# Performance work log

Measured on AMD Instinct MI355X. Metric: run time of the kernel, lower is better.

## Reference

```python
import jax, jax.numpy as jnp
import numpy as np

NUM_EMBEDDINGS = 1024
EMBEDDING_DIM = 64
COMMITMENT_COST = 0.25


def setup_inputs() -> dict:
    key = jax.random.key(0)
    k1, k2 = jax.random.split(key)
    inputs = jax.random.normal(k1, (32, 4096, EMBEDDING_DIM), dtype=jnp.float32)
    lim = 1.0 / NUM_EMBEDDINGS
    embedding = jax.random.uniform(k2, (NUM_EMBEDDINGS, EMBEDDING_DIM),
                                   dtype=jnp.float32, minval=-lim, maxval=lim)
    return {"inputs": inputs, "embedding": embedding}


def reference(inputs, embedding):
    input_shape = inputs.shape
    flat = inputs.reshape(-1, EMBEDDING_DIM)                     # [N, D]
    # Squared euclidean distances via the expanded form (same math as torch cdist trick)
    distances = (jnp.sum(flat ** 2, axis=1, keepdims=True)
                 + jnp.sum(embedding ** 2, axis=1)
                 - 2.0 * flat @ embedding.T)                     # [N, K]
    encoding_indices = jnp.argmin(distances, axis=1)             # [N]
    # one-hot @ embedding == gather of nearest code rows
    quantized = embedding[encoding_indices].reshape(input_shape)
    e_latent_loss = jnp.mean((jax.lax.stop_gradient(quantized) - inputs) ** 2)
    q_latent_loss = jnp.mean((quantized - jax.lax.stop_gradient(inputs)) ** 2)
    loss = q_latent_loss + COMMITMENT_COST * e_latent_loss
    # straight-through estimator
    quantized_st = inputs + jax.lax.stop_gradient(quantized - inputs)
    return loss, quantized_st, encoding_indices[:, None]
```

## Files before the change

### kernel.cpp

```cpp
#include <hip/hip_runtime.h>

#define D 64
#define K 1024
#define NROWS (32 * 4096)
#define NELEM (NROWS * D)
#define COMMIT 0.25f
#define DELTA 1.2e-4f
#define HDELTA 6e-5f
#define RPB 128
#define CHUNK 128
#define EPAD 68

typedef __attribute__((ext_vector_type(8))) short short8v;
typedef __attribute__((ext_vector_type(4))) float f32x4;
typedef unsigned long long u64;

#define FORSLOT8(M) M(0) M(1) M(2) M(3) M(4) M(5) M(6) M(7)

static __device__ __forceinline__ float fence(float v) {
    asm("" : "+v"(v));
    return v;
}

static __device__ __forceinline__ unsigned short f2bf(float f) {
    unsigned u = __float_as_uint(f);
    return (unsigned short)((u + 0x7FFFu + ((u >> 16) & 1u)) >> 16);
}

static __device__ __forceinline__ float np_sumsq64(const float* __restrict__ e) {
    float r[8];
#pragma unroll
    for (int j = 0; j < 8; ++j) r[j] = fence(e[j] * e[j]);
#pragma unroll
    for (int t = 1; t < 8; ++t)
#pragma unroll
        for (int j = 0; j < 8; ++j) r[j] = r[j] + fence(e[8 * t + j] * e[8 * t + j]);
    return ((r[0] + r[1]) + (r[2] + r[3])) + ((r[4] + r[5]) + (r[6] + r[7]));
}

static __device__ __forceinline__ float exact_score(
    const float* __restrict__ xrow, const float* __restrict__ erow, float R,
    float N) {
    float a = 0.0f;
#pragma unroll
    for (int i = 0; i < D; ++i) a = __builtin_fmaf(xrow[i], erow[i], a);
    return (R + N) - 2.0f * a;
}

__global__ void prep_emb_kernel(const float* __restrict__ emb,
                                float* __restrict__ enorm,
                                float* __restrict__ enorm_nh,
                                unsigned short* __restrict__ e_hi,
                                float* __restrict__ loss_slot) {
    int k = blockIdx.x * blockDim.x + threadIdx.x;
    if (k == 0) *loss_slot = 0.0f;
    if (k >= K) return;
    float n = np_sumsq64(emb + k * D);
    enorm[k] = n;
    enorm_nh[k] = -0.5f * n;
    const float* e = emb + k * D;
#pragma unroll
    for (int i = 0; i < D; ++i) e_hi[k * D + i] = f2bf(e[i]);
}

__global__ __launch_bounds__(256, 1) void argmin_kernel(
    const float* __restrict__ x, const float* __restrict__ emb,
    const float* __restrict__ enorm, const float* __restrict__ enorm_nh,
    const unsigned short* __restrict__ e_hi, float* __restrict__ out_q,
    float* __restrict__ idx_f, float* __restrict__ loss_slot) {
    const int tid = threadIdx.x;
    const int l = tid & 63;
    const int w = tid >> 6;
    const int col = l & 15;
    const int koff = (l >> 4) * 8;
    const int blockrow = blockIdx.x * RPB;
    const int wrow = blockrow + w * 32;

    __shared__ unsigned short eB[CHUNK * EPAD];
    __shared__ float nB[CHUNK];
    __shared__ int cnt[RPB];
    __shared__ int clist[RPB][4];
    __shared__ int bidx[RPB];
    __shared__ float wsum[4];

#define DECL_A(rt, h)                                                       \
    short8v Ahi_##rt##_##h;                                                 \
    { const float* p = x + (size_t)(wrow + rt * 16 + col) * D + h * 32 + koff; \
      float4 q0 = *(const float4*)p, q1 = *(const float4*)(p + 4);          \
      Ahi_##rt##_##h[0] = (short)f2bf(q0.x);                                \
      Ahi_##rt##_##h[1] = (short)f2bf(q0.y);                                \
      Ahi_##rt##_##h[2] = (short)f2bf(q0.z);                                \
      Ahi_##rt##_##h[3] = (short)f2bf(q0.w);                                \
      Ahi_##rt##_##h[4] = (short)f2bf(q1.x);                                \
      Ahi_##rt##_##h[5] = (short)f2bf(q1.y);                                \
      Ahi_##rt##_##h[6] = (short)f2bf(q1.z);                                \
      Ahi_##rt##_##h[7] = (short)f2bf(q1.w); }
    DECL_A(0, 0) DECL_A(0, 1) DECL_A(1, 0) DECL_A(1, 1)

#define SLOTROW(s) (((s) / 4) * 16 + (l >> 4) * 4 + ((s) % 4))

#define STAGE(c)                                                            \
    {                                                                       \
        _Pragma("unroll")                                                   \
        for (int i = 0; i < 4; ++i) {                                       \
            int G = tid + i * 256;                 \
            int cd = G >> 3, wi = G & 7;                                    \
            *(short8v*)(&eB[cd * EPAD + wi * 8]) =                          \
                *(const short8v*)(e_hi +                                    \
                    (((size_t)((c) * CHUNK + cd)) << 6) + wi * 8);          \
        }                                                                   \
        if (tid < CHUNK) nB[tid] = enorm_nh[(c) * CHUNK + tid];             \
    }

#define DECL_MA(s) float mA_##s = -3.402823466e+38f;
    FORSLOT8(DECL_MA)
#define MFMA2A(rt, sA, sB, sC, sD)                                          \
    { f32x4 acc = {Nc, Nc, Nc, Nc};                                         \
      acc = __builtin_amdgcn_mfma_f32_16x16x32_bf16(Ahi_##rt##_0, Bhi0, acc, 0, 0, 0); \
      acc = __builtin_amdgcn_mfma_f32_16x16x32_bf16(Ahi_##rt##_1, Bhi1, acc, 0, 0, 0); \
      mA_##sA = fmaxf(mA_##sA, acc[0]);                                     \
      mA_##sB = fmaxf(mA_##sB, acc[1]);                                     \
      mA_##sC = fmaxf(mA_##sC, acc[2]);                                     \
      mA_##sD = fmaxf(mA_##sD, acc[3]); }
    for (int c = 0; c < 8; ++c) {
        __syncthreads();
        STAGE(c)
        __syncthreads();
#pragma unroll 2
        for (int nt = 0; nt < 8; ++nt) {
            const int cc = nt * 16 + col;
            const short8v Bhi0 = *(const short8v*)(&eB[cc * EPAD + koff]);
            const short8v Bhi1 = *(const short8v*)(&eB[cc * EPAD + 32 + koff]);
            const float Nc = nB[cc];
            MFMA2A(0, 0, 1, 2, 3) MFMA2A(1, 4, 5, 6, 7)
        }
    }
#define BFA(s)                                                              \
    mA_##s = fmaxf(mA_##s, __shfl_xor(mA_##s, 1));                          \
    mA_##s = fmaxf(mA_##s, __shfl_xor(mA_##s, 2));                          \
    mA_##s = fmaxf(mA_##s, __shfl_xor(mA_##s, 4));                          \
    mA_##s = fmaxf(mA_##s, __shfl_xor(mA_##s, 8));
    FORSLOT8(BFA)
#define DECL_T(s) const float thr_##s = mA_##s - HDELTA;
    FORSLOT8(DECL_T)
    if (tid < RPB) cnt[tid] = 0;

#define CHK(s, av)                                                          \
    { if ((av) >= thr_##s) {                                                \
          int row = w * 32 + SLOTROW(s);                                    \
          int pos = atomicAdd(&cnt[row], 1);                                \
          if (pos < 4) clist[row][pos] = code;                              \
      } }
#define MFMA2B(rt, sA, sB, sC, sD)                                          \
    { f32x4 acc = {Nc, Nc, Nc, Nc};                                         \
      acc = __builtin_amdgcn_mfma_f32_16x16x32_bf16(Ahi_##rt##_0, Bhi0, acc, 0, 0, 0); \
      acc = __builtin_amdgcn_mfma_f32_16x16x32_bf16(Ahi_##rt##_1, Bhi1, acc, 0, 0, 0); \
      CHK(sA, acc[0]) CHK(sB, acc[1]) CHK(sC, acc[2]) CHK(sD, acc[3]) }
    for (int c = 0; c < 8; ++c) {
        __syncthreads();
        STAGE(c)
        __syncthreads();
#pragma unroll 2
        for (int nt = 0; nt < 8; ++nt) {
            const int cc = nt * 16 + col;
            const short8v Bhi0 = *(const short8v*)(&eB[cc * EPAD + koff]);
            const short8v Bhi1 = *(const short8v*)(&eB[cc * EPAD + 32 + koff]);
            const float Nc = nB[cc];
            const int code = c * CHUNK + cc;
            MFMA2B(0, 0, 1, 2, 3) MFMA2B(1, 4, 5, 6, 7)
        }
    }
    __syncthreads();

    if (tid < RPB) {
        const int row = tid;
        const int n = cnt[row];
        int bk;
        if (n == 1) {
            bk = clist[row][0];
        } else {
            const float* xrow = x + (size_t)(blockrow + row) * D;
            const float R = np_sumsq64(xrow);
            float sb = 3.402823466e+38f;
            int kb = 0x7fffffff;
            if (n <= 4) {
                for (int i = 0; i < n; ++i) {
                    int c = clist[row][i];
                    float s = exact_score(xrow, emb + ((size_t)c << 6), R,
                                          enorm[c]);
                    if (s < sb || (s == sb && c < kb)) { sb = s; kb = c; }
                }
            } else {
                for (int c = 0; c < K; ++c) {
                    float s = exact_score(xrow, emb + ((size_t)c << 6), R,
                                          enorm[c]);
                    if (s < sb || (s == sb && c < kb)) { sb = s; kb = c; }
                }
            }
            bk = kb;
        }
        bidx[row] = bk;
        idx_f[blockrow + row] = (float)bk;
    }
    __syncthreads();

    float lsum = 0.f;
#pragma unroll
    for (int rr = 0; rr < 2; ++rr) {
        const int row = rr * 64 + (tid >> 2);
        const int d0 = (tid & 3) * 16;
        const int bk = bidx[row];
        const float4* xq =
            (const float4*)(x + (size_t)(blockrow + row) * D + d0);
        const float4* eq = (const float4*)(emb + ((size_t)bk << 6) + d0);
        float4* oq = (float4*)(out_q + (size_t)(blockrow + row) * D + d0);
#pragma unroll
        for (int i = 0; i < 4; ++i) {
            float4 xv = xq[i];
            float4 ev = eq[i];
            float dx = ev.x - xv.x, dy = ev.y - xv.y, dz = ev.z - xv.z,
                  dw = ev.w - xv.w;
            float4 o;
            o.x = xv.x + dx;
            o.y = xv.y + dy;
            o.z = xv.z + dz;
            o.w = xv.w + dw;
            oq[i] = o;
            lsum = __builtin_fmaf(dx, dx, lsum);
            lsum = __builtin_fmaf(dy, dy, lsum);
            lsum = __builtin_fmaf(dz, dz, lsum);
            lsum = __builtin_fmaf(dw, dw, lsum);
        }
    }
#pragma unroll
    for (int o = 32; o > 0; o >>= 1) lsum += __shfl_xor(lsum, o);
    if (l == 0) wsum[w] = lsum;
    __syncthreads();
    if (tid == 0)
        atomicAdd(loss_slot, ((wsum[0] + wsum[1]) + (wsum[2] + wsum[3])) *
                                 ((1.0f + COMMIT) / (float)NELEM));
}

extern "C" void kernel_launch(void* const* d_in, const int* in_sizes, int n_in,
                              void* d_out, int out_size, void* d_ws,
                              size_t ws_size, hipStream_t stream) {
    const float* x = (const float*)d_in[0];
    const float* emb = (const float*)d_in[1];

    float* out = (float*)d_out;
    float* loss_slot = out;
    float* out_q = out + 1;
    float* idx_f = out + 1 + NELEM;

    float* enorm = (float*)d_ws;
    float* enorm_nh = (float*)((char*)d_ws + 4096);
    unsigned short* e_hi = (unsigned short*)((char*)d_ws + 8192);

    prep_emb_kernel<<<(K + 255) / 256, 256, 0, stream>>>(emb, enorm, enorm_nh,
                                                         e_hi, loss_slot);
    argmin_kernel<<<NROWS / RPB, 256, 0, stream>>>(x, emb, enorm, enorm_nh,
                                                   e_hi, out_q, idx_f,
                                                   loss_slot);
}
```

Measured before the change: 74.43 us.

## Pre-pad codebook with folded norms and stage via direct global-to-LDS loads

The prep kernel now writes the bf16 codebook already in the padded LDS layout (row stride 68), placing the -0.5*norm float in the pad slots. The argmin kernel stages each chunk with global_load_lds copies straight into shared memory instead of loading through registers, and reads the norm from the padded row, which removes the separate nB array. This is meant to cut VGPR traffic and instruction count in staging. It depends on the layout and byte offsets of the direct-to-LDS copies being correct.

```diff
diff --git a/kernel.cpp b/kernel.cpp
--- a/kernel.cpp
+++ b/kernel.cpp
@@ -10,6 +10,7 @@
 #define RPB 128
 #define CHUNK 128
 #define EPAD 68
+#define CBYTES (CHUNK * EPAD * 2)
 
 typedef __attribute__((ext_vector_type(8))) short short8v;
 typedef __attribute__((ext_vector_type(4))) float f32x4;
@@ -49,25 +50,35 @@
 
 __global__ void prep_emb_kernel(const float* __restrict__ emb,
                                 float* __restrict__ enorm,
-                                float* __restrict__ enorm_nh,
-                                unsigned short* __restrict__ e_hi,
+                                unsigned short* __restrict__ e_pad,
                                 float* __restrict__ loss_slot) {
     int k = blockIdx.x * blockDim.x + threadIdx.x;
     if (k == 0) *loss_slot = 0.0f;
     if (k >= K) return;
     float n = np_sumsq64(emb + k * D);
     enorm[k] = n;
-    enorm_nh[k] = -0.5f * n;
     const float* e = emb + k * D;
-#pragma unroll
-    for (int i = 0; i < D; ++i) e_hi[k * D + i] = f2bf(e[i]);
-}
+    unsigned short* row = e_pad + k * EPAD;
+#pragma unroll
+    for (int i = 0; i < D; ++i) row[i] = f2bf(e[i]);
+    float nh = -0.5f * n;
+    unsigned nb = __float_as_uint(nh);
+    row[64] = (unsigned short)(nb & 0xFFFFu);
+    row[65] = (unsigned short)(nb >> 16);
+    row[66] = 0;
+    row[67] = 0;
+}
+
+#define GLDS(SRC, DST, SZ)                                                  \
+    __builtin_amdgcn_global_load_lds(                                       \
+        (const __attribute__((address_space(1))) unsigned int*)(SRC),       \
+        (__attribute__((address_space(3))) unsigned int*)(DST), SZ, 0, 0)
 
 __global__ __launch_bounds__(256, 1) void argmin_kernel(
     const float* __restrict__ x, const float* __restrict__ emb,
-    const float* __restrict__ enorm, const float* __restrict__ enorm_nh,
-    const unsigned short* __restrict__ e_hi, float* __restrict__ out_q,
-    float* __restrict__ idx_f, float* __restrict__ loss_slot) {
+    const float* __restrict__ enorm, const unsigned short* __restrict__ e_pad,
+    float* __restrict__ out_q, float* __restrict__ idx_f,
+    float* __restrict__ loss_slot) {
     const int tid = threadIdx.x;
     const int l = tid & 63;
     const int w = tid >> 6;
@@ -77,7 +88,6 @@
     const int wrow = blockrow + w * 32;
 
     __shared__ unsigned short eB[CHUNK * EPAD];
-    __shared__ float nB[CHUNK];
     __shared__ int cnt[RPB];
     __shared__ int clist[RPB][4];
     __shared__ int bidx[RPB];
@@ -101,15 +111,15 @@
 
 #define STAGE(c)                                                            \
     {                                                                       \
+        const char* src = (const char*)e_pad + (size_t)(c) * CBYTES;        \
+        char* dst = (char*)eB;                                              \
         _Pragma("unroll")                                                   \
         for (int i = 0; i < 4; ++i) {                                       \
-            int G = tid + i * 256;                 \
-            int cd = G >> 3, wi = G & 7;                                    \
-            *(short8v*)(&eB[cd * EPAD + wi * 8]) =                          \
-                *(const short8v*)(e_hi +                                    \
-                    (((size_t)((c) * CHUNK + cd)) << 6) + wi * 8);          \
+            int off = w * 1024 + i * 4096;                                  \
+            GLDS(src + off + l * 16, dst + off, 16);                        \
         }                                                                   \
-        if (tid < CHUNK) nB[tid] = enorm_nh[(c) * CHUNK + tid];             \
+        { int off4 = 16384 + w * 256;                                       \
+          GLDS(src + off4 + l * 4, dst + off4, 4); }                        \
     }
 
 #define DECL_MA(s) float mA_##s = -3.402823466e+38f;
@@ -131,7 +141,7 @@
             const int cc = nt * 16 + col;
             const short8v Bhi0 = *(const short8v*)(&eB[cc * EPAD + koff]);
             const short8v Bhi1 = *(const short8v*)(&eB[cc * EPAD + 32 + koff]);
-            const float Nc = nB[cc];
+            const float Nc = *(const float*)(&eB[cc * EPAD + 64]);
             MFMA2A(0, 0, 1, 2, 3) MFMA2A(1, 4, 5, 6, 7)
         }
     }
@@ -165,7 +175,7 @@
             const int cc = nt * 16 + col;
             const short8v Bhi0 = *(const short8v*)(&eB[cc * EPAD + koff]);
             const short8v Bhi1 = *(const short8v*)(&eB[cc * EPAD + 32 + koff]);
-            const float Nc = nB[cc];
+            const float Nc = *(const float*)(&eB[cc * EPAD + 64]);
             const int code = c * CHUNK + cc;
             MFMA2B(0, 0, 1, 2, 3) MFMA2B(1, 4, 5, 6, 7)
         }
@@ -253,12 +263,10 @@
     float* idx_f = out + 1 + NELEM;
 
     float* enorm = (float*)d_ws;
-    float* enorm_nh = (float*)((char*)d_ws + 4096);
-    unsigned short* e_hi = (unsigned short*)((char*)d_ws + 8192);
-
-    prep_emb_kernel<<<(K + 255) / 256, 256, 0, stream>>>(emb, enorm, enorm_nh,
-                                                         e_hi, loss_slot);
-    argmin_kernel<<<NROWS / RPB, 256, 0, stream>>>(x, emb, enorm, enorm_nh,
-                                                   e_hi, out_q, idx_f,
-                                                   loss_slot);
-}
+    unsigned short* e_pad = (unsigned short*)((char*)d_ws + 4096);
+
+    prep_emb_kernel<<<(K + 255) / 256, 256, 0, stream>>>(emb, enorm, e_pad,
+                                                         loss_slot);
+    argmin_kernel<<<NROWS / RPB, 256, 0, stream>>>(x, emb, enorm, e_pad,
+                                                   out_q, idx_f, loss_slot);
+}
```

Result: no change. 73.50 us, median of 4 (-1.3%).
